# Kernel optimization log

Hardware: AMD Instinct MI355X
Metric: run time of the kernel (lower is better)

Reference implementation:

```python
import jax, jax.numpy as jnp
import numpy as np

N, E, F_IN, F_EXP, H, C = 8192, 65536, 3247, 7993, 3, 512
HC = H * C
NEG_SLOPE = 0.2


def setup_inputs() -> dict:
    key = jax.random.key(0)
    ks = jax.random.split(key, 40)
    s = 0.02
    rnd = lambda k, *sh: (jax.random.normal(k, sh, jnp.float32) * s)
    d = {}
    d['x'] = jax.random.normal(ks[0], (N, F_IN), jnp.float32)
    d['edge_index'] = jax.random.randint(ks[1], (2, E), 0, N, jnp.int32)
    d['exp'] = jax.random.normal(ks[2], (N, F_EXP), jnp.float32)
    # GATv2 layer 1 (in=3247)
    d['w1l'] = rnd(ks[3], F_IN, HC); d['b1l'] = rnd(ks[4], HC)
    d['w1r'] = rnd(ks[5], F_IN, HC); d['b1r'] = rnd(ks[6], HC)
    d['a1'] = rnd(ks[7], H, C);      d['o1'] = rnd(ks[8], HC)
    # GATv2 layer 2 (in=1536)
    d['w2l'] = rnd(ks[9], HC, HC);  d['b2l'] = rnd(ks[10], HC)
    d['w2r'] = rnd(ks[11], HC, HC); d['b2r'] = rnd(ks[12], HC)
    d['a2'] = rnd(ks[13], H, C);     d['o2'] = rnd(ks[14], HC)
    # GATv2 layer 3 (in=1536)
    d['w3l'] = rnd(ks[15], HC, HC); d['b3l'] = rnd(ks[16], HC)
    d['w3r'] = rnd(ks[17], HC, HC); d['b3r'] = rnd(ks[18], HC)
    d['a3'] = rnd(ks[19], H, C);     d['o3'] = rnd(ks[20], HC)
    # encoder: 7993 -> 4000 -> 1500 -> 512
    d['e1w'] = rnd(ks[21], F_EXP, 4000); d['e1b'] = rnd(ks[22], 4000)
    d['e2w'] = rnd(ks[23], 4000, 1500);  d['e2b'] = rnd(ks[24], 1500)
    d['e3w'] = rnd(ks[25], 1500, 512);   d['e3b'] = rnd(ks[26], 512)
    # head: 2048 -> 1024 -> 512 -> 1
    d['l1w'] = rnd(ks[27], HC + 512, 1024); d['l1b'] = rnd(ks[28], 1024)
    d['l2w'] = rnd(ks[29], 1024, 512);      d['l2b'] = rnd(ks[30], 512)
    d['l3w'] = rnd(ks[31], 512, 1);         d['l3b'] = rnd(ks[32], 1)
    return d


def gatv2(h, src, dst, wl, bl, wr, br, att, out_bias):
    # PyG GATv2Conv: e_ij = a^T LeakyReLU(W_l h_j + W_r h_i), softmax over j per target i,
    # out_i = sum_j alpha_ij * (W_l h_j), concat heads, + bias.
    xl = (h @ wl + bl).reshape(N, H, C)
    xr = (h @ wr + br).reshape(N, H, C)
    e = jax.nn.leaky_relu(xl[src] + xr[dst], NEG_SLOPE)      # [E', H, C]
    logit = jnp.einsum('ehc,hc->eh', e, att)                  # [E', H]
    m = jax.ops.segment_max(logit, dst, num_segments=N)       # [N, H]
    p = jnp.exp(logit - m[dst])
    z = jax.ops.segment_sum(p, dst, num_segments=N)
    alpha = p / z[dst]                                        # segment softmax
    out = jax.ops.segment_sum(alpha[:, :, None] * xl[src], dst, num_segments=N)
    return out.reshape(N, HC) + out_bias


def reference(x, edge_index, exp,
              w1l, b1l, w1r, b1r, a1, o1,
              w2l, b2l, w2r, b2r, a2, o2,
              w3l, b3l, w3r, b3r, a3, o3,
              e1w, e1b, e2w, e2b, e3w, e3b,
              l1w, l1b, l2w, l2b, l3w, l3b):
    loops = jnp.arange(N, dtype=edge_index.dtype)
    src = jnp.concatenate([edge_index[0], loops])  # add_self_loops=True (PyG default)
    dst = jnp.concatenate([edge_index[1], loops])
    h = jax.nn.relu(gatv2(x, src, dst, w1l, b1l, w1r, b1r, a1, o1))
    h = jax.nn.relu(gatv2(h, src, dst, w2l, b2l, w2r, b2r, a2, o2))
    h = jax.nn.relu(gatv2(h, src, dst, w3l, b3l, w3r, b3r, a3, o3))
    cell = jax.nn.relu(exp @ e1w + e1b)
    cell = jax.nn.relu(cell @ e2w + e2b)
    cell = cell @ e3w + e3b
    z = jnp.concatenate([h, cell], axis=1)  # [N, 2048]
    z = jax.nn.relu(z @ l1w + l1b)
    z = jax.nn.relu(z @ l2w + l2b)
    return z @ l3w + l3b  # [N, 1]
```

## Files before the change

kernel.cpp:

```cpp
#include <hip/hip_runtime.h>
#include <stdint.h>

#define NN 8192
#define NE 65536
#define ET (NE + NN)
#define F_IN   3247
#define F_IN_P 3264
#define F_EXP   7993
#define F_EXP_P 8000

typedef __attribute__((ext_vector_type(8))) short bf16x8;
typedef __attribute__((ext_vector_type(4))) float f32x4;

typedef const __attribute__((address_space(1))) void gvoid_t;
typedef __attribute__((address_space(3))) void lvoid_t;

__device__ __forceinline__ float bf2f(uint16_t u) {
  union { uint32_t i; float f; } v; v.i = ((uint32_t)u) << 16; return v.f;
}
__device__ __forceinline__ uint16_t f2bf(float f) {
  union { float f; uint32_t i; } v; v.f = f;
  uint32_t r = v.i + 0x7fffu + ((v.i >> 16) & 1u);
  return (uint16_t)(r >> 16);
}

__device__ __forceinline__ void gld_lds16(const void* g, void* l) {
  __builtin_amdgcn_global_load_lds((gvoid_t*)g, (lvoid_t*)l, 16, 0, 0);
}

#define SBAR() __builtin_amdgcn_sched_barrier(0)
#define BARRIER() do { SBAR(); __builtin_amdgcn_s_barrier(); SBAR(); } while (0)
#define VMCNT(n) asm volatile("s_waitcnt vmcnt(" #n ")" ::: "memory")
#define MFMA16(a, b, c) __builtin_amdgcn_mfma_f32_16x16x32_bf16(a, b, c, 0, 0, 0)

__device__ __forceinline__ void stage4(const char* src, char* dst, size_t Kb) {
#pragma unroll
  for (int j = 0; j < 4; ++j)
    gld_lds16(src + (size_t)(j * 64) * Kb, dst + j * 8192);
}

#define KTILE(T, BUF)                                                          \
  do {                                                                         \
    const char* aB_  = smem + (BUF) + arow;                                    \
    const char* bB_  = smem + 65536 + (BUF) + brow_o;                          \
    const char* aBn_ = smem + ((BUF) ^ 32768) + arow;                          \
    const bool nls = ((T) + 2 < nk);                                           \
    const bool nlr = ((T) + 1 < nk);                                           \
                        \
    if (nlr) { VMCNT(8); } else { VMCNT(0); }                                  \
    _Pragma("unroll")                                                          \
    for (int n = 0; n < 2; ++n) {                                              \
      b01[n * 2]     = *(const bf16x8*)(bB_ + n * 2048 + sw0);                 \
      b01[n * 2 + 1] = *(const bf16x8*)(bB_ + n * 2048 + sw1);                 \
    }                                                                          \
    _Pragma("unroll")                                                          \
    for (int n = 0; n < 2; ++n) {                                              \
      b23[n * 2]     = *(const bf16x8*)(bB_ + (n + 2) * 2048 + sw0);           \
      b23[n * 2 + 1] = *(const bf16x8*)(bB_ + (n + 2) * 2048 + sw1);           \
    }                                                                          \
    SBAR();                                                                    \
    __builtin_amdgcn_s_setprio(1);                                             \
    _Pragma("unroll")                                                          \
    for (int m = 0; m < 4; ++m)                                                \
      _Pragma("unroll")                                                        \
      for (int n = 0; n < 2; ++n) {                                            \
        acc[m][n] = MFMA16(a03[m * 2],     b01[n * 2],     acc[m][n]);         \
        acc[m][n] = MFMA16(a03[m * 2 + 1], b01[n * 2 + 1], acc[m][n]);         \
      }                                                                        \
    __builtin_amdgcn_s_setprio(0);                                             \
    BARRIER();                                                                 \
                                        \
    _Pragma("unroll")                                                          \
    for (int m = 0; m < 4; ++m) {                                              \
      a47[m * 2]     = *(const bf16x8*)(aB_ + (m + 4) * 2048 + sw0);           \
      a47[m * 2 + 1] = *(const bf16x8*)(aB_ + (m + 4) * 2048 + sw1);           \
    }                                                                          \
    SBAR();                                                                    \
    __builtin_amdgcn_s_setprio(1);                                             \
    _Pragma("unroll")                                                          \
    for (int m = 0; m < 4; ++m)                                                \
      _Pragma("unroll")                                                        \
      for (int n = 0; n < 2; ++n) {                                            \
        acc[m][n + 2] = MFMA16(a03[m * 2],     b23[n * 2],     acc[m][n + 2]); \
        acc[m][n + 2] = MFMA16(a03[m * 2 + 1], b23[n * 2 + 1], acc[m][n + 2]); \
      }                                                                        \
    __builtin_amdgcn_s_setprio(0);                                             \
    BARRIER();                                                                 \
                       \
    if (nls) stage4(pA + (size_t)((T) + 2) * 128, sA + (BUF), Kb);             \
    _Pragma("unroll")                                                          \
    for (int n = 0; n < 2; ++n) {                                              \
      b01[n * 2]     = *(const bf16x8*)(bB_ + n * 2048 + sw0);                 \
      b01[n * 2 + 1] = *(const bf16x8*)(bB_ + n * 2048 + sw1);                 \
    }                                                                          \
    SBAR();                                                                    \
    __builtin_amdgcn_s_setprio(1);                                             \
    _Pragma("unroll")                                                          \
    for (int m = 0; m < 4; ++m)                                                \
      _Pragma("unroll")                                                        \
      for (int n = 0; n < 2; ++n) {                                            \
        acc[m + 4][n + 2] = MFMA16(a47[m * 2],     b23[n * 2],     acc[m + 4][n + 2]); \
        acc[m + 4][n + 2] = MFMA16(a47[m * 2 + 1], b23[n * 2 + 1], acc[m + 4][n + 2]); \
      }                                                                        \
    __builtin_amdgcn_s_setprio(0);                                             \
    BARRIER();                                                                 \
       \
    if (nls)      { VMCNT(10); }                                               \
    else if (nlr) { VMCNT(4); }                                                \
    if (nlr) {                                                                 \
      _Pragma("unroll")                                                        \
      for (int m = 0; m < 4; ++m) {                                            \
        a03[m * 2]     = *(const bf16x8*)(aBn_ + m * 2048 + sw0);              \
        a03[m * 2 + 1] = *(const bf16x8*)(aBn_ + m * 2048 + sw1);              \
      }                                                                        \
    }                                                                          \
    if (nls) stage4(pB + (size_t)((T) + 2) * 128, sB + (BUF), Kb);             \
    SBAR();                                                                    \
    __builtin_amdgcn_s_setprio(1);                                             \
    _Pragma("unroll")                                                          \
    for (int m = 0; m < 4; ++m)                                                \
      _Pragma("unroll")                                                        \
      for (int n = 0; n < 2; ++n) {                                            \
        acc[m + 4][n] = MFMA16(a47[m * 2],     b01[n * 2],     acc[m + 4][n]); \
        acc[m + 4][n] = MFMA16(a47[m * 2 + 1], b01[n * 2 + 1], acc[m + 4][n]); \
      }                                                                        \
    __builtin_amdgcn_s_setprio(0);                                             \
    BARRIER();                                                                 \
  } while (0)

__global__ __launch_bounds__(512, 2)
void gemm256(const uint16_t* __restrict__ A, const uint16_t* __restrict__ Bt,
             const float* __restrict__ bias, int biasN, int relu,
             uint16_t* __restrict__ C, int Kp, int ldc, int nbn)
{
  extern __shared__ char smem[];
  const int tid = threadIdx.x;
  const int w = tid >> 6, lane = tid & 63;
  const int wr = w >> 2, wc = w & 3;
  const int fr = lane & 15, g = lane >> 4;

  const int nwg = (int)gridDim.x;
  const int id = (int)blockIdx.x;
  const int q = nwg >> 3, r = nwg & 7;
  const int xcd = id & 7, idx = id >> 3;
  const int wg = (xcd < r ? xcd * (q + 1) : r * (q + 1) + (xcd - r) * q) + idx;
  const int brow = (wg / nbn) * 256, bcol = (wg % nbn) * 256;

  const size_t Kb = (size_t)Kp * 2;

  const int srow = tid >> 3;
  const int sswz = ((tid & 7) ^ (srow & 7)) * 16;
  const char* pA = (const char*)A + (size_t)(brow + srow) * Kb + sswz;
  const char* pB = (const char*)Bt + (size_t)(bcol + srow) * Kb + sswz;
  char* sA = smem + w * 1024;
  char* sB = smem + 65536 + w * 1024;

  const int sw0 = (g ^ (fr & 7)) * 16;
  const int sw1 = ((g + 4) ^ (fr & 7)) * 16;
  const int arow = (wr * 128 + fr) * 128;
  const int brow_o = (wc * 64 + fr) * 128;

  f32x4 acc[8][4];
#pragma unroll
  for (int m = 0; m < 8; ++m)
#pragma unroll
    for (int n = 0; n < 4; ++n) acc[m][n] = (f32x4){0.f, 0.f, 0.f, 0.f};
  bf16x8 a03[8], a47[8], b01[4], b23[4];

  stage4(pA, sA, Kb);
  stage4(pB, sB, Kb);
  stage4(pA + 128, sA + 32768, Kb);
  stage4(pB + 128, sB + 32768, Kb);
  VMCNT(8);
  BARRIER();
  {
    const char* aB = smem + arow;
#pragma unroll
    for (int m = 0; m < 4; ++m) {
      a03[m * 2]     = *(const bf16x8*)(aB + m * 2048 + sw0);
      a03[m * 2 + 1] = *(const bf16x8*)(aB + m * 2048 + sw1);
    }
  }
  SBAR();

  const int nk = Kp >> 6;
  for (int t = 0; t < nk; t += 2) {
    KTILE(t, 0);
    if (t + 1 < nk) KTILE(t + 1, 32768);
  }

#pragma unroll
  for (int m = 0; m < 8; ++m) {
    const int row = brow + wr * 128 + m * 16 + g * 4;
#pragma unroll
    for (int n = 0; n < 4; ++n) {
      const int col = bcol + wc * 64 + n * 16 + fr;
      const float bv = (col < biasN) ? bias[col] : 0.f;
#pragma unroll
      for (int j = 0; j < 4; ++j) {
        float v = acc[m][n][j] + bv;
        if (relu) v = fmaxf(v, 0.f);
        C[(size_t)(row + j) * ldc + col] = f2bf(v);
      }
    }
  }
}

__global__ __launch_bounds__(256)
void gemm_bt(const uint16_t* __restrict__ A, const uint16_t* __restrict__ Bt,
             const float* __restrict__ bias, int biasN, int relu,
             uint16_t* __restrict__ C, int Kp, int ldc)
{
  __shared__ uint16_t As[128 * 32];
  __shared__ uint16_t Bs[128 * 32];
  const int tid  = threadIdx.x;
  const int wave = tid >> 6, lane = tid & 63;
  const int brow = blockIdx.x * 128, bcol = blockIdx.y * 128;
  const int wr = wave >> 1, wc = wave & 1;
  const int fr = lane & 15, g = lane >> 4;

  f32x4 acc[4][4];
#pragma unroll
  for (int m = 0; m < 4; ++m)
#pragma unroll
    for (int n = 0; n < 4; ++n) acc[m][n] = (f32x4){0.f, 0.f, 0.f, 0.f};

  const int rA = tid >> 2;
  const int kc = (tid & 3) * 8;
  const uint16_t* aptr = A  + (size_t)(brow + rA) * Kp + kc;
  const uint16_t* bptr = Bt + (size_t)(bcol + rA) * Kp + kc;
  char* ldsA = (char*)As + wave * 1024;
  char* ldsB = (char*)Bs + wave * 1024;
  const size_t rowskip = (size_t)64 * Kp;

  const int nk = Kp >> 5;
  for (int kt = 0; kt < nk; ++kt) {
    __syncthreads();
    gld_lds16(aptr,           ldsA);
    gld_lds16(aptr + rowskip, ldsA + 4096);
    gld_lds16(bptr,           ldsB);
    gld_lds16(bptr + rowskip, ldsB + 4096);
    aptr += 32; bptr += 32;
    __syncthreads();

    bf16x8 af[4], bfr[4];
#pragma unroll
    for (int m = 0; m < 4; ++m)
      af[m] = *(const bf16x8*)&As[(wr * 64 + m * 16 + fr) * 32 + g * 8];
#pragma unroll
    for (int n = 0; n < 4; ++n)
      bfr[n] = *(const bf16x8*)&Bs[(wc * 64 + n * 16 + fr) * 32 + g * 8];
#pragma unroll
    for (int m = 0; m < 4; ++m)
#pragma unroll
      for (int n = 0; n < 4; ++n)
        acc[m][n] = MFMA16(af[m], bfr[n], acc[m][n]);
  }

#pragma unroll
  for (int m = 0; m < 4; ++m) {
    const int row = brow + wr * 64 + m * 16 + g * 4;
#pragma unroll
    for (int n = 0; n < 4; ++n) {
      const int col = bcol + wc * 64 + n * 16 + fr;
      const float bv = (col < biasN) ? bias[col] : 0.f;
#pragma unroll
      for (int j = 0; j < 4; ++j) {
        float v = acc[m][n][j] + bv;
        if (relu) v = fmaxf(v, 0.f);
        C[(size_t)(row + j) * ldc + col] = f2bf(v);
      }
    }
  }
}

__global__ __launch_bounds__(256)
void cvt_pad(const float* __restrict__ in, uint16_t* __restrict__ out, int cols, int colsPad)
{
  const int r = blockIdx.y;
  const int c = (blockIdx.x * 256 + threadIdx.x) * 2;
  if (c >= colsPad) return;
  const float* ip = in + (size_t)r * cols;
  const float v0 = (c < cols)     ? ip[c]     : 0.f;
  const float v1 = (c + 1 < cols) ? ip[c + 1] : 0.f;
  const uint32_t pk = (uint32_t)f2bf(v0) | ((uint32_t)f2bf(v1) << 16);
  *(uint32_t*)(out + (size_t)r * colsPad + c) = pk;
}

__global__ __launch_bounds__(256)
void transpose_w(const float* __restrict__ W, uint16_t* __restrict__ Wt,
                 int K, int N, int Kp, int Np)
{
  __shared__ float t[32][33];
  const int tx = threadIdx.x, ty = threadIdx.y;
  const int k0 = blockIdx.x * 32, n0 = blockIdx.y * 32;
#pragma unroll
  for (int j = 0; j < 4; ++j) {
    const int k = k0 + ty + j * 8, n = n0 + tx;
    t[ty + j * 8][tx] = (k < K && n < N) ? W[(size_t)k * N + n] : 0.f;
  }
  __syncthreads();
#pragma unroll
  for (int j = 0; j < 4; ++j) {
    const int n = n0 + ty + j * 8, k = k0 + tx;
    Wt[(size_t)n * Kp + k] = f2bf(t[tx][ty + j * 8]);
  }
}

__global__ void concat_bias(const float* __restrict__ bl, const float* __restrict__ br,
                            float* __restrict__ out)
{
  const int i = blockIdx.x * 256 + threadIdx.x;
  if (i < 1536) out[i] = bl[i];
  else if (i < 3072) out[i] = br[i - 1536];
}

__global__ void count_deg(const int* __restrict__ ei, int* __restrict__ counts)
{
  const int e = blockIdx.x * 256 + threadIdx.x;
  if (e >= ET) return;
  const int d = (e < NE) ? ei[NE + e] : (e - NE);
  atomicAdd(&counts[d], 1);
}

__global__ __launch_bounds__(1024)
void scan_deg(const int* __restrict__ counts, int* __restrict__ row_start, int* __restrict__ cursor)
{
  __shared__ int part[1024];
  const int tid = threadIdx.x;
  int loc[8], pre[8], s = 0;
#pragma unroll
  for (int j = 0; j < 8; ++j) { loc[j] = counts[tid * 8 + j]; pre[j] = s; s += loc[j]; }
  part[tid] = s;
  __syncthreads();
  for (int o = 1; o < 1024; o <<= 1) {
    const int v = part[tid];
    const int a = (tid >= o) ? part[tid - o] : 0;
    __syncthreads();
    part[tid] = v + a;
    __syncthreads();
  }
  const int excl = part[tid] - s;
#pragma unroll
  for (int j = 0; j < 8; ++j) {
    const int v = excl + pre[j];
    row_start[tid * 8 + j] = v;
    cursor[tid * 8 + j]    = v;
  }
  if (tid == 1023) row_start[8192] = excl + s;
}

__global__ void scatter_e(const int* __restrict__ ei, int* __restrict__ cursor,
                          int* __restrict__ csr_src, int* __restrict__ csr_dst)
{
  const int e = blockIdx.x * 256 + threadIdx.x;
  if (e >= ET) return;
  const int sx = (e < NE) ? ei[e]      : (e - NE);
  const int d  = (e < NE) ? ei[NE + e] : (e - NE);
  const int pos = atomicAdd(&cursor[d], 1);
  csr_src[pos] = sx;
  csr_dst[pos] = d;
}

__global__ __launch_bounds__(256)
void gat_fused(const uint16_t* __restrict__ xlr, int ld,
               const int* __restrict__ csr_src, const int* __restrict__ row_start,
               const float* __restrict__ att, const float* __restrict__ ob,
               uint16_t* __restrict__ out, int ldc)
{
  const int node = (blockIdx.x << 2) + (threadIdx.x >> 6);
  const int lane = threadIdx.x & 63;

  float av[3][8], xr[3][8];
  const bf16x8* pr = (const bf16x8*)(xlr + (size_t)node * ld + 1536);
#pragma unroll
  for (int h = 0; h < 3; ++h) {
    const float4 a0 = *(const float4*)(att + h * 512 + lane * 8);
    const float4 a1 = *(const float4*)(att + h * 512 + lane * 8 + 4);
    av[h][0] = a0.x; av[h][1] = a0.y; av[h][2] = a0.z; av[h][3] = a0.w;
    av[h][4] = a1.x; av[h][5] = a1.y; av[h][6] = a1.z; av[h][7] = a1.w;
    const bf16x8 v = pr[h * 64 + lane];
#pragma unroll
    for (int j = 0; j < 8; ++j) xr[h][j] = bf2f((uint16_t)v[j]);
  }

  float m[3] = {-1e30f, -1e30f, -1e30f};
  float z[3] = {0.f, 0.f, 0.f};
  float acc[3][8];
#pragma unroll
  for (int h = 0; h < 3; ++h)
#pragma unroll
    for (int j = 0; j < 8; ++j) acc[h][j] = 0.f;

  const int s0 = row_start[node], s1 = row_start[node + 1];
  for (int s = s0; s < s1; ++s) {
    const bf16x8* pl = (const bf16x8*)(xlr + (size_t)csr_src[s] * ld);
    bf16x8 vl[3];
#pragma unroll
    for (int h = 0; h < 3; ++h) vl[h] = pl[h * 64 + lane];

    float hacc[3];
#pragma unroll
    for (int h = 0; h < 3; ++h) {
      float sacc = 0.f;
#pragma unroll
      for (int j = 0; j < 8; ++j) {
        float v = bf2f((uint16_t)vl[h][j]) + xr[h][j];
        v = v > 0.f ? v : 0.2f * v;
        sacc += v * av[h][j];
      }
      hacc[h] = sacc;
    }
#pragma unroll
    for (int o = 32; o; o >>= 1) {
      hacc[0] += __shfl_xor(hacc[0], o);
      hacc[1] += __shfl_xor(hacc[1], o);
      hacc[2] += __shfl_xor(hacc[2], o);
    }
#pragma unroll
    for (int h = 0; h < 3; ++h) {
      const float nm = fmaxf(m[h], hacc[h]);
      const float sc = __expf(m[h] - nm);
      const float p  = __expf(hacc[h] - nm);
      z[h] = z[h] * sc + p;
#pragma unroll
      for (int j = 0; j < 8; ++j)
        acc[h][j] = acc[h][j] * sc + p * bf2f((uint16_t)vl[h][j]);
      m[h] = nm;
    }
  }

#pragma unroll
  for (int h = 0; h < 3; ++h) {
    const float rz = 1.f / z[h];
    const float4 b0 = *(const float4*)(ob + h * 512 + lane * 8);
    const float4 b1 = *(const float4*)(ob + h * 512 + lane * 8 + 4);
    float bv[8] = {b0.x, b0.y, b0.z, b0.w, b1.x, b1.y, b1.z, b1.w};
    bf16x8 pk;
#pragma unroll
    for (int j = 0; j < 8; ++j) {
      const float v = fmaxf(acc[h][j] * rz + bv[j], 0.f);
      pk[j] = (short)f2bf(v);
    }
    *(bf16x8*)(out + (size_t)node * ldc + h * 512 + lane * 8) = pk;
  }
}

__global__ __launch_bounds__(256)
void final_dot(const uint16_t* __restrict__ z2, const float* __restrict__ w,
               const float* __restrict__ b, float* __restrict__ out)
{
  const int row  = blockIdx.x * 4 + (threadIdx.x >> 6);
  const int lane = threadIdx.x & 63;
  const uint16_t* p = z2 + (size_t)row * 512;
  float s = 0.f;
#pragma unroll
  for (int j = 0; j < 8; ++j) { const int c = lane + j * 64; s += bf2f(p[c]) * w[c]; }
#pragma unroll
  for (int o = 32; o; o >>= 1) s += __shfl_xor(s, o);
  if (lane == 0) out[row] = s + b[0];
}

extern "C" void kernel_launch(void* const* d_in, const int* in_sizes, int n_in,
                              void* d_out, int out_size, void* d_ws, size_t ws_size,
                              hipStream_t stream)
{
  (void)in_sizes; (void)n_in; (void)out_size; (void)ws_size;

  const float* x    = (const float*)d_in[0];
  const int*   ei   = (const int*)  d_in[1];
  const float* expm = (const float*)d_in[2];
  const float* w1l = (const float*)d_in[3];  const float* b1l = (const float*)d_in[4];
  const float* w1r = (const float*)d_in[5];  const float* b1r = (const float*)d_in[6];
  const float* a1  = (const float*)d_in[7];  const float* o1  = (const float*)d_in[8];
  const float* w2l = (const float*)d_in[9];  const float* b2l = (const float*)d_in[10];
  const float* w2r = (const float*)d_in[11]; const float* b2r = (const float*)d_in[12];
  const float* a2  = (const float*)d_in[13]; const float* o2  = (const float*)d_in[14];
  const float* w3l = (const float*)d_in[15]; const float* b3l = (const float*)d_in[16];
  const float* w3r = (const float*)d_in[17]; const float* b3r = (const float*)d_in[18];
  const float* a3  = (const float*)d_in[19]; const float* o3  = (const float*)d_in[20];
  const float* e1w = (const float*)d_in[21]; const float* e1b = (const float*)d_in[22];
  const float* e2w = (const float*)d_in[23]; const float* e2b = (const float*)d_in[24];
  const float* e3w = (const float*)d_in[25]; const float* e3b = (const float*)d_in[26];
  const float* l1w = (const float*)d_in[27]; const float* l1b = (const float*)d_in[28];
  const float* l2w = (const float*)d_in[29]; const float* l2b = (const float*)d_in[30];
  const float* l3w = (const float*)d_in[31]; const float* l3b = (const float*)d_in[32];
  float* out = (float*)d_out;

  hipFuncSetAttribute((const void*)gemm256, hipFuncAttributeMaxDynamicSharedMemorySize, 131072);

  char* ws = (char*)d_ws;
  size_t off = 0;
  auto take = [&](size_t b) { char* p = ws + off; off += (b + 255) & ~(size_t)255; return p; };

  int*      counts    = (int*)take((size_t)NN * 4);
  int*      row_start = (int*)take((size_t)(NN + 1) * 4);
  int*      cursor    = (int*)take((size_t)NN * 4);
  int*      csr_src   = (int*)take((size_t)ET * 4);
  int*      csr_dst   = (int*)take((size_t)ET * 4);
  float*    bc1       = (float*)take(3072 * 4);
  float*    bc2       = (float*)take(3072 * 4);
  float*    bc3       = (float*)take(3072 * 4);
  uint16_t* zbuf      = (uint16_t*)take((size_t)NN * 2048 * 2);
  char*     regA      = take((size_t)NN * F_EXP_P * 2);
  char*     regW      = take((size_t)4096 * F_EXP_P * 2);
  char*     regC      = take((size_t)NN * 4096 * 2 + (size_t)NN * 1536 * 2);

  uint16_t* xbf   = (uint16_t*)regA;
  uint16_t* expbf = (uint16_t*)regA;
  uint16_t* wT    = (uint16_t*)regW;
  uint16_t* xlr   = (uint16_t*)regC;
  uint16_t* hbuf  = (uint16_t*)(regC + (size_t)NN * 3072 * 2);
  uint16_t* cell1 = (uint16_t*)regC;
  uint16_t* cell2 = (uint16_t*)(regC + (size_t)NN * 4096 * 2);
  uint16_t* zz1   = (uint16_t*)regC;
  uint16_t* zz2   = (uint16_t*)(regC + (size_t)NN * 1024 * 2);

  hipMemsetAsync(counts, 0, (size_t)NN * 4, stream);
  count_deg<<<(ET + 255) / 256, 256, 0, stream>>>(ei, counts);
  scan_deg<<<1, 1024, 0, stream>>>(counts, row_start, cursor);
  scatter_e<<<(ET + 255) / 256, 256, 0, stream>>>(ei, cursor, csr_src, csr_dst);
  concat_bias<<<12, 256, 0, stream>>>(b1l, b1r, bc1);
  concat_bias<<<12, 256, 0, stream>>>(b2l, b2r, bc2);
  concat_bias<<<12, 256, 0, stream>>>(b3l, b3r, bc3);

  cvt_pad<<<dim3((F_IN_P / 2 + 255) / 256, NN), 256, 0, stream>>>(x, xbf, F_IN, F_IN_P);
  transpose_w<<<dim3(F_IN_P / 32, 1536 / 32), dim3(32, 8), 0, stream>>>(w1l, wT, F_IN, 1536, F_IN_P, 1536);
  transpose_w<<<dim3(F_IN_P / 32, 1536 / 32), dim3(32, 8), 0, stream>>>(w1r, wT + (size_t)1536 * F_IN_P, F_IN, 1536, F_IN_P, 1536);
  gemm256<<<32 * 12, 512, 131072, stream>>>(xbf, wT, bc1, 3072, 0, xlr, F_IN_P, 3072, 12);
  gat_fused<<<NN / 4, 256, 0, stream>>>(xlr, 3072, csr_src, row_start, a1, o1, hbuf, 1536);

  transpose_w<<<dim3(48, 48), dim3(32, 8), 0, stream>>>(w2l, wT, 1536, 1536, 1536, 1536);
  transpose_w<<<dim3(48, 48), dim3(32, 8), 0, stream>>>(w2r, wT + (size_t)1536 * 1536, 1536, 1536, 1536, 1536);
  gemm256<<<32 * 12, 512, 131072, stream>>>(hbuf, wT, bc2, 3072, 0, xlr, 1536, 3072, 12);
  gat_fused<<<NN / 4, 256, 0, stream>>>(xlr, 3072, csr_src, row_start, a2, o2, hbuf, 1536);

  transpose_w<<<dim3(48, 48), dim3(32, 8), 0, stream>>>(w3l, wT, 1536, 1536, 1536, 1536);
  transpose_w<<<dim3(48, 48), dim3(32, 8), 0, stream>>>(w3r, wT + (size_t)1536 * 1536, 1536, 1536, 1536, 1536);
  gemm256<<<32 * 12, 512, 131072, stream>>>(hbuf, wT, bc3, 3072, 0, xlr, 1536, 3072, 12);
  gat_fused<<<NN / 4, 256, 0, stream>>>(xlr, 3072, csr_src, row_start, a3, o3, zbuf, 2048);

  cvt_pad<<<dim3((F_EXP_P / 2 + 255) / 256, NN), 256, 0, stream>>>(expm, expbf, F_EXP, F_EXP_P);
  transpose_w<<<dim3(F_EXP_P / 32, 4096 / 32), dim3(32, 8), 0, stream>>>(e1w, wT, F_EXP, 4000, F_EXP_P, 4096);
  gemm256<<<32 * 16, 512, 131072, stream>>>(expbf, wT, e1b, 4000, 1, cell1, F_EXP_P, 4096, 16);
  transpose_w<<<dim3(4096 / 32, 1536 / 32), dim3(32, 8), 0, stream>>>(e2w, wT, 4000, 1500, 4096, 1536);
  gemm256<<<32 * 6, 512, 131072, stream>>>(cell1, wT, e2b, 1500, 1, cell2, 4096, 1536, 6);
  transpose_w<<<dim3(1536 / 32, 512 / 32), dim3(32, 8), 0, stream>>>(e3w, wT, 1500, 512, 1536, 512);
  gemm_bt<<<dim3(64, 4), 256, 0, stream>>>(cell2, wT, e3b, 512, 0, zbuf + 1536, 1536, 2048);

  transpose_w<<<dim3(2048 / 32, 1024 / 32), dim3(32, 8), 0, stream>>>(l1w, wT, 2048, 1024, 2048, 1024);
  gemm_bt<<<dim3(64, 8), 256, 0, stream>>>(zbuf, wT, l1b, 1024, 1, zz1, 2048, 1024);
  transpose_w<<<dim3(1024 / 32, 512 / 32), dim3(32, 8), 0, stream>>>(l2w, wT, 1024, 512, 1024, 512);
  gemm_bt<<<dim3(64, 4), 256, 0, stream>>>(zz1, wT, l2b, 512, 1, zz2, 1024, 512);
  final_dot<<<NN / 4, 256, 0, stream>>>(zz2, l3w, l3b, out);
}
```

Before: 1.466 ms.

## Restructure GEMM k-tile inner loop into K-half phases with smaller register fragments

```diff
diff --git a/kernel.cpp b/kernel.cpp
--- a/kernel.cpp
+++ b/kernel.cpp
@@ -30,6 +30,7 @@
 
 #define SBAR() __builtin_amdgcn_sched_barrier(0)
 #define BARRIER() do { SBAR(); __builtin_amdgcn_s_barrier(); SBAR(); } while (0)
+#define LGKM0() do { asm volatile("s_waitcnt lgkmcnt(0)" ::: "memory"); SBAR(); } while (0)
 #define VMCNT(n) asm volatile("s_waitcnt vmcnt(" #n ")" ::: "memory")
 #define MFMA16(a, b, c) __builtin_amdgcn_mfma_f32_16x16x32_bf16(a, b, c, 0, 0, 0)
 
@@ -44,86 +45,73 @@
     const char* aB_  = smem + (BUF) + arow;                                    \
     const char* bB_  = smem + 65536 + (BUF) + brow_o;                          \
     const char* aBn_ = smem + ((BUF) ^ 32768) + arow;                          \
+    const char* bBn_ = smem + 65536 + ((BUF) ^ 32768) + brow_o;                \
     const bool nls = ((T) + 2 < nk);                                           \
     const bool nlr = ((T) + 1 < nk);                                           \
-                        \
-    if (nlr) { VMCNT(8); } else { VMCNT(0); }                                  \
-    _Pragma("unroll")                                                          \
-    for (int n = 0; n < 2; ++n) {                                              \
-      b01[n * 2]     = *(const bf16x8*)(bB_ + n * 2048 + sw0);                 \
-      b01[n * 2 + 1] = *(const bf16x8*)(bB_ + n * 2048 + sw1);                 \
-    }                                                                          \
-    _Pragma("unroll")                                                          \
-    for (int n = 0; n < 2; ++n) {                                              \
-      b23[n * 2]     = *(const bf16x8*)(bB_ + (n + 2) * 2048 + sw0);           \
-      b23[n * 2 + 1] = *(const bf16x8*)(bB_ + (n + 2) * 2048 + sw1);           \
-    }                                                                          \
+     \
+    _Pragma("unroll")                                                          \
+    for (int m = 0; m < 4; ++m)                                                \
+      a1f[m] = *(const bf16x8*)(aB_ + (m + 4) * 2048 + sw0);                   \
     SBAR();                                                                    \
     __builtin_amdgcn_s_setprio(1);                                             \
     _Pragma("unroll")                                                          \
     for (int m = 0; m < 4; ++m)                                                \
       _Pragma("unroll")                                                        \
-      for (int n = 0; n < 2; ++n) {                                            \
-        acc[m][n] = MFMA16(a03[m * 2],     b01[n * 2],     acc[m][n]);         \
-        acc[m][n] = MFMA16(a03[m * 2 + 1], b01[n * 2 + 1], acc[m][n]);         \
-      }                                                                        \
+      for (int n = 0; n < 4; ++n)                                              \
+        acc[m][n] = MFMA16(a0f[m], b0f[n], acc[m][n]);                         \
     __builtin_amdgcn_s_setprio(0);                                             \
-    BARRIER();                                                                 \
-                                        \
-    _Pragma("unroll")                                                          \
-    for (int m = 0; m < 4; ++m) {                                              \
-      a47[m * 2]     = *(const bf16x8*)(aB_ + (m + 4) * 2048 + sw0);           \
-      a47[m * 2 + 1] = *(const bf16x8*)(aB_ + (m + 4) * 2048 + sw1);           \
-    }                                                                          \
+    SBAR();                                                                    \
+     \
+    _Pragma("unroll")                                                          \
+    for (int m = 0; m < 4; ++m)                                                \
+      a0f[m] = *(const bf16x8*)(aB_ + m * 2048 + sw1);                         \
+    _Pragma("unroll")                                                          \
+    for (int n = 0; n < 4; ++n)                                                \
+      b1f[n] = *(const bf16x8*)(bB_ + n * 2048 + sw1);                         \
     SBAR();                                                                    \
     __builtin_amdgcn_s_setprio(1);                                             \
     _Pragma("unroll")                                                          \
     for (int m = 0; m < 4; ++m)                                                \
       _Pragma("unroll")                                                        \
-      for (int n = 0; n < 2; ++n) {                                            \
-        acc[m][n + 2] = MFMA16(a03[m * 2],     b23[n * 2],     acc[m][n + 2]); \
-        acc[m][n + 2] = MFMA16(a03[m * 2 + 1], b23[n * 2 + 1], acc[m][n + 2]); \
-      }                                                                        \
+      for (int n = 0; n < 4; ++n)                                              \
+        acc[m + 4][n] = MFMA16(a1f[m], b0f[n], acc[m + 4][n]);                 \
     __builtin_amdgcn_s_setprio(0);                                             \
+    LGKM0();                 \
     BARRIER();                                                                 \
-                       \
-    if (nls) stage4(pA + (size_t)((T) + 2) * 128, sA + (BUF), Kb);             \
-    _Pragma("unroll")                                                          \
-    for (int n = 0; n < 2; ++n) {                                              \
-      b01[n * 2]     = *(const bf16x8*)(bB_ + n * 2048 + sw0);                 \
-      b01[n * 2 + 1] = *(const bf16x8*)(bB_ + n * 2048 + sw1);                 \
-    }                                                                          \
+             \
+    if (nls) stage4(pB + (size_t)((T) + 2) * 128, sB + (BUF), Kb);             \
+    _Pragma("unroll")                                                          \
+    for (int m = 0; m < 4; ++m)                                                \
+      a1f[m] = *(const bf16x8*)(aB_ + (m + 4) * 2048 + sw1);                   \
     SBAR();                                                                    \
     __builtin_amdgcn_s_setprio(1);                                             \
     _Pragma("unroll")                                                          \
     for (int m = 0; m < 4; ++m)                                                \
       _Pragma("unroll")                                                        \
-      for (int n = 0; n < 2; ++n) {                                            \
-        acc[m + 4][n + 2] = MFMA16(a47[m * 2],     b23[n * 2],     acc[m + 4][n + 2]); \
-        acc[m + 4][n + 2] = MFMA16(a47[m * 2 + 1], b23[n * 2 + 1], acc[m + 4][n + 2]); \
-      }                                                                        \
+      for (int n = 0; n < 4; ++n)                                              \
+        acc[m][n] = MFMA16(a0f[m], b1f[n], acc[m][n]);                         \
     __builtin_amdgcn_s_setprio(0);                                             \
+    if (nls)      { VMCNT(4); }                                                \
+    else if (nlr) { VMCNT(0); }                                                \
+    LGKM0();                     \
     BARRIER();                                                                 \
-       \
-    if (nls)      { VMCNT(10); }                                               \
-    else if (nlr) { VMCNT(4); }                                                \
+                             \
     if (nlr) {                                                                 \
       _Pragma("unroll")                                                        \
-      for (int m = 0; m < 4; ++m) {                                            \
-        a03[m * 2]     = *(const bf16x8*)(aBn_ + m * 2048 + sw0);              \
-        a03[m * 2 + 1] = *(const bf16x8*)(aBn_ + m * 2048 + sw1);              \
-      }                                                                        \
+      for (int m = 0; m < 4; ++m)                                              \
+        a0f[m] = *(const bf16x8*)(aBn_ + m * 2048 + sw0);                      \
+      _Pragma("unroll")                                                        \
+      for (int n = 0; n < 4; ++n)                                              \
+        b0f[n] = *(const bf16x8*)(bBn_ + n * 2048 + sw0);                      \
     }                                                                          \
-    if (nls) stage4(pB + (size_t)((T) + 2) * 128, sB + (BUF), Kb);             \
+    if (nls) stage4(pA + (size_t)((T) + 2) * 128, sA + (BUF), Kb);             \
     SBAR();                                                                    \
     __builtin_amdgcn_s_setprio(1);                                             \
     _Pragma("unroll")                                                          \
     for (int m = 0; m < 4; ++m)                                                \
       _Pragma("unroll")                                                        \
-      for (int n = 0; n < 2; ++n) {                                            \
-        acc[m + 4][n] = MFMA16(a47[m * 2],     b01[n * 2],     acc[m + 4][n]); \
-        acc[m + 4][n] = MFMA16(a47[m * 2 + 1], b01[n * 2 + 1], acc[m + 4][n]); \
-      }                                                                        \
+      for (int n = 0; n < 4; ++n)                                              \
+        acc[m + 4][n] = MFMA16(a1f[m], b1f[n], acc[m + 4][n]);                 \
     __builtin_amdgcn_s_setprio(0);                                             \
     BARRIER();                                                                 \
   } while (0)
@@ -165,7 +153,7 @@
   for (int m = 0; m < 8; ++m)
 #pragma unroll
     for (int n = 0; n < 4; ++n) acc[m][n] = (f32x4){0.f, 0.f, 0.f, 0.f};
-  bf16x8 a03[8], a47[8], b01[4], b23[4];
+  bf16x8 a0f[4], a1f[4], b0f[4], b1f[4];
 
   stage4(pA, sA, Kb);
   stage4(pB, sB, Kb);
@@ -173,14 +161,12 @@
   stage4(pB + 128, sB + 32768, Kb);
   VMCNT(8);
   BARRIER();
-  {
-    const char* aB = smem + arow;
-#pragma unroll
-    for (int m = 0; m < 4; ++m) {
-      a03[m * 2]     = *(const bf16x8*)(aB + m * 2048 + sw0);
-      a03[m * 2 + 1] = *(const bf16x8*)(aB + m * 2048 + sw1);
-    }
-  }
+#pragma unroll
+  for (int m = 0; m < 4; ++m)
+    a0f[m] = *(const bf16x8*)(smem + arow + m * 2048 + sw0);
+#pragma unroll
+  for (int n = 0; n < 4; ++n)
+    b0f[n] = *(const bf16x8*)(smem + 65536 + brow_o + n * 2048 + sw0);
   SBAR();
 
   const int nk = Kp >> 6;
```

Result: no change. 1.444 ms (-1.6%).
